# Optimization experiments

Measured on AMD Instinct MI355X. Metric: run time of the kernel, lower is better.

The kernel has to match this reference:

```python
import jax, jax.numpy as jnp
import numpy as np

B, S, H, UNITS = 32, 2048, 1024, 1024


def setup_inputs() -> dict:
    key = jax.random.key(0)
    ks = jax.random.split(key, 5)
    scale = 1.0 / np.sqrt(H)
    return {
        "query": jax.random.normal(ks[0], (B, H), dtype=jnp.float32),
        "values": jax.random.normal(ks[1], (B, S, H), dtype=jnp.float32),
        "W1": jax.random.normal(ks[2], (H, UNITS), dtype=jnp.float32) * scale,
        "b1": jnp.zeros((UNITS,), dtype=jnp.float32),
        "W2": jax.random.normal(ks[3], (H, UNITS), dtype=jnp.float32) * scale,
        "b2": jnp.zeros((UNITS,), dtype=jnp.float32),
        "V": jax.random.normal(ks[4], (UNITS, 1), dtype=jnp.float32) * (1.0 / np.sqrt(UNITS)),
        "bV": jnp.zeros((1,), dtype=jnp.float32),
    }


def reference(query, values, W1, b1, W2, b2, V, bV):
    # W1(values): [B,S,U]; W2(query): [B,1,U] broadcast over S
    proj_v = jnp.einsum("bsh,hu->bsu", values, W1) + b1
    proj_q = (query @ W2 + b2)[:, None, :]
    score = jnp.tanh(proj_v + proj_q) @ V + bV          # [B,S,1]
    attention_weights = jax.nn.softmax(score, axis=1)   # softmax over seq
    context_vector = jnp.sum(attention_weights * values, axis=1)  # [B,H]
    return (attention_weights, context_vector)
```

## Files before the change

### kernel.cpp

```cpp
#include <hip/hip_runtime.h>
#include <hip/hip_bf16.h>
#include <stdint.h>

#define B_ 32
#define S_ 2048
#define H_ 1024
#define U_ 1024

typedef __attribute__((ext_vector_type(8))) short short8;
typedef __attribute__((ext_vector_type(4))) float f32x4;

#define AS1 __attribute__((address_space(1)))
#define AS3 __attribute__((address_space(3)))
#define FENCE __builtin_amdgcn_sched_barrier(0)
#define VMC(n) asm volatile("s_waitcnt vmcnt(" #n ")" ::: "memory")
#define LGKM0 asm volatile("s_waitcnt lgkmcnt(0)" ::: "memory")

__device__ __forceinline__ unsigned short f2bf(float f) {
  unsigned int u = __float_as_uint(f);
  u += 0x7fffu + ((u >> 16) & 1u);
  return (unsigned short)(u >> 16);
}

__global__ void k_transpose_w1(const float* __restrict__ W1, unsigned short* __restrict__ W1T) {
  __shared__ float tile[64][65];
  const int tx = threadIdx.x, ty = threadIdx.y;
  const int u0 = blockIdx.x * 64, h0 = blockIdx.y * 64;
#pragma unroll
  for (int i = 0; i < 16; ++i) {
    int hl = ty + i * 4;
    tile[hl][tx] = W1[(size_t)(h0 + hl) * U_ + (u0 + tx)];
  }
  __syncthreads();
#pragma unroll
  for (int i = 0; i < 16; ++i) {
    int ul = ty + i * 4;
    W1T[(size_t)(u0 + ul) * H_ + (h0 + tx)] = f2bf(tile[tx][ul]);
  }
}

__global__ void k_b1q(const float* __restrict__ query, const float* __restrict__ W2,
                      const float* __restrict__ b1, const float* __restrict__ b2,
                      float* __restrict__ b1q) {
  const int b = blockIdx.y;
  const int u = blockIdx.x * 256 + threadIdx.x;
  float acc = b1[u] + b2[u];
  const float* q = query + b * H_;
#pragma unroll 8
  for (int h = 0; h < H_; ++h) acc += q[h] * W2[(size_t)h * U_ + u];
  b1q[b * U_ + u] = acc;
}

#define BMT 256
#define BNT 256
#define BKT 64
#define NTILE 16

__global__ __launch_bounds__(512, 2)
void k_fused_score(const float* __restrict__ values, const unsigned short* __restrict__ W1T,
                   const float* __restrict__ b1q, const float* __restrict__ V,
                   float* __restrict__ score_part) {
  __shared__ __align__(16) unsigned char smem[131072];
  unsigned short* Abuf = (unsigned short*)smem;
  unsigned short* Bbuf = (unsigned short*)(smem + 65536);
  float* scorebuf = (float*)smem;

  const int tid = threadIdx.x;
  const int g = blockIdx.x;
  const int seq = (g & 7) * 128 + (g >> 3);
  const int bn = seq & 3;
  const int bm = seq >> 2;

  const int lane = tid & 63, wid = tid >> 6;
  const int wm = wid >> 2, wn = wid & 3;
  const int u0 = bn * BNT;

  const int arow = tid >> 2;
  const int acp  = (tid & 3) * 2;
  const float* aBase = values + (size_t)(bm * BMT) * H_;

  const int l15 = lane & 15, l16 = lane >> 4, l7 = lane & 7;
  const int pA0 = (wm * 128 + l15) * 64 + ((0 + l16) ^ l7) * 8;
  const int pA1 = (wm * 128 + l15) * 64 + ((4 + l16) ^ l7) * 8;
  const int pB0 = (wn * 64 + l15) * 64 + ((0 + l16) ^ l7) * 8;
  const int pB1 = (wn * 64 + l15) * 64 + ((4 + l16) ^ l7) * 8;

  f32x4 acc[8][4];
#pragma unroll
  for (int mf = 0; mf < 8; ++mf)
#pragma unroll
    for (int nf = 0; nf < 4; ++nf) acc[mf][nf] = (f32x4){0.f, 0.f, 0.f, 0.f};

  float4 ar0[4], ar1[4];
  short8 af[4], bfv[8];

#define ISSUE_A(reg, tt, h) { \
    const float4* ap_ = (const float4*)(aBase + (size_t)((h) * 128 + arow) * H_ + (tt) * 64 + acp * 8); \
    reg[0] = ap_[0]; reg[1] = ap_[1]; reg[2] = ap_[2]; reg[3] = ap_[3]; }

#define ISSUE_B(tt, dd, h) { \
    _Pragma("unroll") \
    for (int j_ = 0; j_ < 2; ++j_) { \
      const int pbase_ = (h) * 1024 + (wid * 2 + j_) * 64; \
      const int p_ = pbase_ + lane; \
      const int nr_ = p_ >> 3; \
      const int lc_ = (p_ & 7) ^ (nr_ & 7); \
      const unsigned short* src_ = W1T + (size_t)(u0 + nr_) * H_ + (tt) * 64 + lc_ * 8; \
      __builtin_amdgcn_global_load_lds((const AS1 void*)src_, (AS3 void*)&Bbuf[(dd) * 16384 + pbase_ * 8], 16, 0, 0); } }

#define WRITE_A(reg, dd, h) { \
    short8 w0_, w1_; \
    w0_[0]=f2bf(reg[0].x); w0_[1]=f2bf(reg[0].y); w0_[2]=f2bf(reg[0].z); w0_[3]=f2bf(reg[0].w); \
    w0_[4]=f2bf(reg[1].x); w0_[5]=f2bf(reg[1].y); w0_[6]=f2bf(reg[1].z); w0_[7]=f2bf(reg[1].w); \
    w1_[0]=f2bf(reg[2].x); w1_[1]=f2bf(reg[2].y); w1_[2]=f2bf(reg[2].z); w1_[3]=f2bf(reg[2].w); \
    w1_[4]=f2bf(reg[3].x); w1_[5]=f2bf(reg[3].y); w1_[6]=f2bf(reg[3].z); w1_[7]=f2bf(reg[3].w); \
    const int rl_ = (h) * 128 + arow; \
    *(short8*)&Abuf[(dd) * 16384 + rl_ * 64 + ((acp ^ (rl_ & 7)) << 3)] = w0_; \
    *(short8*)&Abuf[(dd) * 16384 + rl_ * 64 + (((acp + 1) ^ (rl_ & 7)) << 3)] = w1_; }

#define READ_AF(q) \
    af[0] = *(const short8*)&Abuf[dA + pA0 + (2 * (q) + 0) * 1024]; \
    af[1] = *(const short8*)&Abuf[dA + pA1 + (2 * (q) + 0) * 1024]; \
    af[2] = *(const short8*)&Abuf[dA + pA0 + (2 * (q) + 1) * 1024]; \
    af[3] = *(const short8*)&Abuf[dA + pA1 + (2 * (q) + 1) * 1024];

#define PHASE_TAIL(q) \
    FENCE; \
    __builtin_amdgcn_s_barrier(); \
    LGKM0; \
    FENCE; \
    __builtin_amdgcn_s_setprio(1); \
    _Pragma("unroll") \
    for (int nf_ = 0; nf_ < 4; ++nf_) { \
      acc[2*(q)+0][nf_] = __builtin_amdgcn_mfma_f32_16x16x32_bf16(af[0], bfv[2*nf_+0], acc[2*(q)+0][nf_], 0, 0, 0); \
      acc[2*(q)+0][nf_] = __builtin_amdgcn_mfma_f32_16x16x32_bf16(af[1], bfv[2*nf_+1], acc[2*(q)+0][nf_], 0, 0, 0); \
      acc[2*(q)+1][nf_] = __builtin_amdgcn_mfma_f32_16x16x32_bf16(af[2], bfv[2*nf_+0], acc[2*(q)+1][nf_], 0, 0, 0); \
      acc[2*(q)+1][nf_] = __builtin_amdgcn_mfma_f32_16x16x32_bf16(af[3], bfv[2*nf_+1], acc[2*(q)+1][nf_], 0, 0, 0); \
    } \
    __builtin_amdgcn_s_setprio(0); \
    FENCE; \
    __builtin_amdgcn_s_barrier();

  ISSUE_A(ar0, 0, 0);
  ISSUE_A(ar1, 0, 1);
  ISSUE_B(0, 0, 0);
  ISSUE_B(0, 0, 1);
  VMC(8);  WRITE_A(ar0, 0, 0);
  VMC(4);  WRITE_A(ar1, 0, 1);
  FENCE;
  ISSUE_A(ar0, 1, 0);
  FENCE;
  VMC(4);
  LGKM0;
  __builtin_amdgcn_s_barrier();

  for (int t = 0; t < NTILE; ++t) {
    const int d = t & 1, dn = d ^ 1;
    const int n  = (t + 1 < NTILE) ? (t + 1) : (NTILE - 1);
    const int n2 = (t + 2 < NTILE) ? (t + 2) : (NTILE - 1);
    const int dA = d * 16384;
    const int dB = d * 16384;

    READ_AF(0);
    bfv[0] = *(const short8*)&Bbuf[dB + pB0 + 0 * 1024];
    bfv[1] = *(const short8*)&Bbuf[dB + pB1 + 0 * 1024];
    bfv[2] = *(const short8*)&Bbuf[dB + pB0 + 1 * 1024];
    bfv[3] = *(const short8*)&Bbuf[dB + pB1 + 1 * 1024];
    bfv[4] = *(const short8*)&Bbuf[dB + pB0 + 2 * 1024];
    bfv[5] = *(const short8*)&Bbuf[dB + pB1 + 2 * 1024];
    bfv[6] = *(const short8*)&Bbuf[dB + pB0 + 3 * 1024];
    bfv[7] = *(const short8*)&Bbuf[dB + pB1 + 3 * 1024];
    ISSUE_A(ar1, n, 1);
    ISSUE_B(n, dn, 0);
    PHASE_TAIL(0);

    READ_AF(1);
    ISSUE_B(n, dn, 1);
    PHASE_TAIL(1);

    READ_AF(2);
    VMC(8);
    WRITE_A(ar0, dn, 0);
    PHASE_TAIL(2);

    READ_AF(3);
    VMC(4);
    WRITE_A(ar1, dn, 1);
    FENCE;
    ISSUE_A(ar0, n2, 0);
    FENCE;
    VMC(4);
    PHASE_TAIL(3);
  }

  __syncthreads();
  const int b_blk = bm >> 3;
  float bqv[4], vvv[4];
#pragma unroll
  for (int nf = 0; nf < 4; ++nf) {
    const int ug = u0 + wn * 64 + nf * 16 + l15;
    bqv[nf] = b1q[b_blk * U_ + ug];
    vvv[nf] = V[ug];
  }
  float rp[8][4];
#pragma unroll
  for (int mf = 0; mf < 8; ++mf)
#pragma unroll
    for (int j = 0; j < 4; ++j) rp[mf][j] = 0.f;
#pragma unroll
  for (int nf = 0; nf < 4; ++nf)
#pragma unroll
    for (int mf = 0; mf < 8; ++mf) {
      const f32x4 c = acc[mf][nf];
#pragma unroll
      for (int j = 0; j < 4; ++j) {
        const float x = c[j] + bqv[nf];
        const float e = __expf(2.f * x);
        const float tt = 1.f - 2.f / (e + 1.f);
        rp[mf][j] += tt * vvv[nf];
      }
    }
#pragma unroll
  for (int mf = 0; mf < 8; ++mf)
#pragma unroll
    for (int j = 0; j < 4; ++j) {
      float v = rp[mf][j];
      v += __shfl_xor(v, 1);
      v += __shfl_xor(v, 2);
      v += __shfl_xor(v, 4);
      v += __shfl_xor(v, 8);
      rp[mf][j] = v;
    }
  if (l15 == 0) {
#pragma unroll
    for (int mf = 0; mf < 8; ++mf)
#pragma unroll
      for (int j = 0; j < 4; ++j)
        scorebuf[(wm * 128 + mf * 16 + l16 * 4 + j) * 4 + wn] = rp[mf][j];
  }
  __syncthreads();
  if (tid < BMT) {
    const float s = scorebuf[tid * 4 + 0] + scorebuf[tid * 4 + 1] +
                    scorebuf[tid * 4 + 2] + scorebuf[tid * 4 + 3];
    score_part[(size_t)bn * (B_ * S_) + bm * BMT + tid] = s;
  }
}

__global__ void k_softmax(const float* __restrict__ sp, float* __restrict__ aw) {
  __shared__ float red[8];
  const int b = blockIdx.x, tid = threadIdx.x;
  const int BS = B_ * S_;
  float x[8];
  float m = -1e30f;
#pragma unroll
  for (int i = 0; i < 8; ++i) {
    const int s = b * S_ + tid + i * 256;
    x[i] = sp[s] + sp[BS + s] + sp[2 * BS + s] + sp[3 * BS + s];
    m = fmaxf(m, x[i]);
  }
#pragma unroll
  for (int off = 32; off; off >>= 1) m = fmaxf(m, __shfl_xor(m, off));
  if ((tid & 63) == 0) red[tid >> 6] = m;
  __syncthreads();
  m = fmaxf(fmaxf(red[0], red[1]), fmaxf(red[2], red[3]));
  float e[8];
  float sum = 0.f;
#pragma unroll
  for (int i = 0; i < 8; ++i) { e[i] = __expf(x[i] - m); sum += e[i]; }
#pragma unroll
  for (int off = 32; off; off >>= 1) sum += __shfl_xor(sum, off);
  __syncthreads();
  if ((tid & 63) == 0) red[4 + (tid >> 6)] = sum;
  __syncthreads();
  sum = red[4] + red[5] + red[6] + red[7];
  const float inv = 1.f / sum;
#pragma unroll
  for (int i = 0; i < 8; ++i) aw[b * S_ + tid + i * 256] = e[i] * inv;
}

__global__ void k_ctx_partial(const float* __restrict__ values, const float* __restrict__ aw,
                              float* __restrict__ part) {
  __shared__ float a_s[128];
  const int b = blockIdx.y, sc = blockIdx.x, tid = threadIdx.x;
  if (tid < 128) a_s[tid] = aw[b * S_ + sc * 128 + tid];
  __syncthreads();
  const float4* vp = (const float4*)values + (size_t)(b * S_ + sc * 128) * (H_ / 4) + tid;
  float4 acc = {0.f, 0.f, 0.f, 0.f};
#pragma unroll 4
  for (int i = 0; i < 128; ++i) {
    const float4 v = vp[(size_t)i * (H_ / 4)];
    const float a = a_s[i];
    acc.x += a * v.x; acc.y += a * v.y; acc.z += a * v.z; acc.w += a * v.w;
  }
  ((float4*)part)[(size_t)(b * 16 + sc) * (H_ / 4) + tid] = acc;
}

__global__ void k_ctx_combine(const float* __restrict__ part, float* __restrict__ ctx) {
  const int b = blockIdx.x, tid = threadIdx.x;
  float4 s = {0.f, 0.f, 0.f, 0.f};
#pragma unroll
  for (int c = 0; c < 16; ++c) {
    const float4 v = ((const float4*)part)[(size_t)(b * 16 + c) * (H_ / 4) + tid];
    s.x += v.x; s.y += v.y; s.z += v.z; s.w += v.w;
  }
  ((float4*)ctx)[b * (H_ / 4) + tid] = s;
}

extern "C" void kernel_launch(void* const* d_in, const int* in_sizes, int n_in,
                              void* d_out, int out_size, void* d_ws, size_t ws_size,
                              hipStream_t stream) {
  const float* query  = (const float*)d_in[0];
  const float* values = (const float*)d_in[1];
  const float* W1     = (const float*)d_in[2];
  const float* b1     = (const float*)d_in[3];
  const float* W2     = (const float*)d_in[4];
  const float* b2     = (const float*)d_in[5];
  const float* V      = (const float*)d_in[6];

  char* ws = (char*)d_ws;
  unsigned short* W1T = (unsigned short*)ws;
  float* b1q   = (float*)(ws + 2u * 1024u * 1024u);
  float* spart = (float*)(ws + 2u * 1024u * 1024u + 128u * 1024u);
  float* cpart = (float*)(ws + 2u * 1024u * 1024u + 128u * 1024u + 1024u * 1024u);

  float* aw  = (float*)d_out;
  float* ctx = aw + B_ * S_;

  hipLaunchKernelGGL(k_transpose_w1, dim3(16, 16), dim3(64, 4), 0, stream, W1, W1T);
  hipLaunchKernelGGL(k_b1q,          dim3(4, 32),  dim3(256),   0, stream, query, W2, b1, b2, b1q);
  hipLaunchKernelGGL(k_fused_score,  dim3(1024),   dim3(512),   0, stream, values, W1T, b1q, V, spart);
  hipLaunchKernelGGL(k_softmax,      dim3(32),     dim3(256),   0, stream, spart, aw);
  hipLaunchKernelGGL(k_ctx_partial,  dim3(16, 32), dim3(256),   0, stream, values, aw, cpart);
  hipLaunchKernelGGL(k_ctx_combine,  dim3(32),     dim3(256),   0, stream, cpart, ctx);
}
```

Baseline: 343.7 us.

## Pre-convert values to bf16 and stage A tiles via direct global-to-LDS loads

When the workspace is large enough, a separate kernel converts the full values tensor to bf16. The GEMM then loads A tiles straight into LDS with global_load_lds, like B, instead of loading fp32 into registers and converting. The MFMA phase ordering is also restructured to reuse B fragments across four M fragments. This adds a full extra pass over values (256MB read plus 128MB write) in exchange for halving GEMM A traffic and removing in-loop conversion. Whether that path runs depends on the workspace size.

```diff
diff --git a/kernel.cpp b/kernel.cpp
--- a/kernel.cpp
+++ b/kernel.cpp
@@ -20,6 +20,18 @@
   unsigned int u = __float_as_uint(f);
   u += 0x7fffu + ((u >> 16) & 1u);
   return (unsigned short)(u >> 16);
+}
+
+__global__ void k_cvt(const float* __restrict__ v, unsigned short* __restrict__ o) {
+  const size_t n = (size_t)B_ * S_ * H_;
+  const size_t stride = (size_t)gridDim.x * blockDim.x * 8;
+  for (size_t i = ((size_t)blockIdx.x * blockDim.x + threadIdx.x) * 8; i < n; i += stride) {
+    float4 a = *(const float4*)(v + i), b = *(const float4*)(v + i + 4);
+    short8 w;
+    w[0]=f2bf(a.x); w[1]=f2bf(a.y); w[2]=f2bf(a.z); w[3]=f2bf(a.w);
+    w[4]=f2bf(b.x); w[5]=f2bf(b.y); w[6]=f2bf(b.z); w[7]=f2bf(b.w);
+    *(short8*)(o + i) = w;
+  }
 }
 
 __global__ void k_transpose_w1(const float* __restrict__ W1, unsigned short* __restrict__ W1T) {
@@ -53,13 +65,13 @@
 
 #define BMT 256
 #define BNT 256
-#define BKT 64
 #define NTILE 16
 
+template<bool CVT>
 __global__ __launch_bounds__(512, 2)
-void k_fused_score(const float* __restrict__ values, const unsigned short* __restrict__ W1T,
-                   const float* __restrict__ b1q, const float* __restrict__ V,
-                   float* __restrict__ score_part) {
+void k_fused_score(const float* __restrict__ valsf, const unsigned short* __restrict__ vbf,
+                   const unsigned short* __restrict__ W1T, const float* __restrict__ b1q,
+                   const float* __restrict__ V, float* __restrict__ score_part) {
   __shared__ __align__(16) unsigned char smem[131072];
   unsigned short* Abuf = (unsigned short*)smem;
   unsigned short* Bbuf = (unsigned short*)(smem + 65536);
@@ -75,16 +87,15 @@
   const int wm = wid >> 2, wn = wid & 3;
   const int u0 = bn * BNT;
 
-  const int arow = tid >> 2;
-  const int acp  = (tid & 3) * 2;
-  const float* aBase = values + (size_t)(bm * BMT) * H_;
-
   const int l15 = lane & 15, l16 = lane >> 4, l7 = lane & 7;
   const int pA0 = (wm * 128 + l15) * 64 + ((0 + l16) ^ l7) * 8;
   const int pA1 = (wm * 128 + l15) * 64 + ((4 + l16) ^ l7) * 8;
   const int pB0 = (wn * 64 + l15) * 64 + ((0 + l16) ^ l7) * 8;
   const int pB1 = (wn * 64 + l15) * 64 + ((4 + l16) ^ l7) * 8;
 
+  const int lcs = (lane & 7) ^ ((lane >> 3) & 7);
+  const int arow = tid >> 2, acp = (tid & 3) * 2;
+
   f32x4 acc[8][4];
 #pragma unroll
   for (int mf = 0; mf < 8; ++mf)
@@ -92,23 +103,29 @@
     for (int nf = 0; nf < 4; ++nf) acc[mf][nf] = (f32x4){0.f, 0.f, 0.f, 0.f};
 
   float4 ar0[4], ar1[4];
-  short8 af[4], bfv[8];
-
-#define ISSUE_A(reg, tt, h) { \
-    const float4* ap_ = (const float4*)(aBase + (size_t)((h) * 128 + arow) * H_ + (tt) * 64 + acp * 8); \
-    reg[0] = ap_[0]; reg[1] = ap_[1]; reg[2] = ap_[2]; reg[3] = ap_[3]; }
-
-#define ISSUE_B(tt, dd, h) { \
+  short8 af_[4], bv[4];
+
+#define STAGE_A(tt, dd, h) { \
     _Pragma("unroll") \
     for (int j_ = 0; j_ < 2; ++j_) { \
-      const int pbase_ = (h) * 1024 + (wid * 2 + j_) * 64; \
-      const int p_ = pbase_ + lane; \
+      const int p_ = (h) * 1024 + (wid * 2 + j_) * 64 + lane; \
       const int nr_ = p_ >> 3; \
-      const int lc_ = (p_ & 7) ^ (nr_ & 7); \
-      const unsigned short* src_ = W1T + (size_t)(u0 + nr_) * H_ + (tt) * 64 + lc_ * 8; \
-      __builtin_amdgcn_global_load_lds((const AS1 void*)src_, (AS3 void*)&Bbuf[(dd) * 16384 + pbase_ * 8], 16, 0, 0); } }
-
-#define WRITE_A(reg, dd, h) { \
+      const unsigned short* s_ = vbf + (size_t)(bm * BMT + nr_) * H_ + (tt) * 64 + lcs * 8; \
+      __builtin_amdgcn_global_load_lds((const AS1 void*)s_, (AS3 void*)&Abuf[(dd) * 16384 + p_ * 8], 16, 0, 0); } }
+
+#define STAGE_B(tt, dd, h) { \
+    _Pragma("unroll") \
+    for (int j_ = 0; j_ < 2; ++j_) { \
+      const int p_ = (h) * 1024 + (wid * 2 + j_) * 64 + lane; \
+      const int nr_ = p_ >> 3; \
+      const unsigned short* s_ = W1T + (size_t)(u0 + nr_) * H_ + (tt) * 64 + lcs * 8; \
+      __builtin_amdgcn_global_load_lds((const AS1 void*)s_, (AS3 void*)&Bbuf[(dd) * 16384 + p_ * 8], 16, 0, 0); } }
+
+#define ISSUE_AR(reg, tt, h) { \
+    const float4* ap_ = (const float4*)(valsf + (size_t)(bm * BMT + (h) * 128 + arow) * H_ + (tt) * 64 + acp * 8); \
+    reg[0] = ap_[0]; reg[1] = ap_[1]; reg[2] = ap_[2]; reg[3] = ap_[3]; }
+
+#define WRITE_AR(reg, dd, h) { \
     short8 w0_, w1_; \
     w0_[0]=f2bf(reg[0].x); w0_[1]=f2bf(reg[0].y); w0_[2]=f2bf(reg[0].z); w0_[3]=f2bf(reg[0].w); \
     w0_[4]=f2bf(reg[1].x); w0_[5]=f2bf(reg[1].y); w0_[6]=f2bf(reg[1].z); w0_[7]=f2bf(reg[1].w); \
@@ -118,79 +135,84 @@
     *(short8*)&Abuf[(dd) * 16384 + rl_ * 64 + ((acp ^ (rl_ & 7)) << 3)] = w0_; \
     *(short8*)&Abuf[(dd) * 16384 + rl_ * 64 + (((acp + 1) ^ (rl_ & 7)) << 3)] = w1_; }
 
-#define READ_AF(q) \
-    af[0] = *(const short8*)&Abuf[dA + pA0 + (2 * (q) + 0) * 1024]; \
-    af[1] = *(const short8*)&Abuf[dA + pA1 + (2 * (q) + 0) * 1024]; \
-    af[2] = *(const short8*)&Abuf[dA + pA0 + (2 * (q) + 1) * 1024]; \
-    af[3] = *(const short8*)&Abuf[dA + pA1 + (2 * (q) + 1) * 1024];
-
-#define PHASE_TAIL(q) \
-    FENCE; \
-    __builtin_amdgcn_s_barrier(); \
-    LGKM0; \
-    FENCE; \
-    __builtin_amdgcn_s_setprio(1); \
+#define READ_AF(PA, MH) \
+    af_[0] = *(const short8*)&Abuf[dA + (PA) + ((MH) * 4 + 0) * 1024]; \
+    af_[1] = *(const short8*)&Abuf[dA + (PA) + ((MH) * 4 + 1) * 1024]; \
+    af_[2] = *(const short8*)&Abuf[dA + (PA) + ((MH) * 4 + 2) * 1024]; \
+    af_[3] = *(const short8*)&Abuf[dA + (PA) + ((MH) * 4 + 3) * 1024];
+
+#define READ_BV(PB) \
+    bv[0] = *(const short8*)&Bbuf[dB + (PB)]; \
+    bv[1] = *(const short8*)&Bbuf[dB + (PB) + 1024]; \
+    bv[2] = *(const short8*)&Bbuf[dB + (PB) + 2048]; \
+    bv[3] = *(const short8*)&Bbuf[dB + (PB) + 3072];
+
+#define MFMA16(MH) \
     _Pragma("unroll") \
     for (int nf_ = 0; nf_ < 4; ++nf_) { \
-      acc[2*(q)+0][nf_] = __builtin_amdgcn_mfma_f32_16x16x32_bf16(af[0], bfv[2*nf_+0], acc[2*(q)+0][nf_], 0, 0, 0); \
-      acc[2*(q)+0][nf_] = __builtin_amdgcn_mfma_f32_16x16x32_bf16(af[1], bfv[2*nf_+1], acc[2*(q)+0][nf_], 0, 0, 0); \
-      acc[2*(q)+1][nf_] = __builtin_amdgcn_mfma_f32_16x16x32_bf16(af[2], bfv[2*nf_+0], acc[2*(q)+1][nf_], 0, 0, 0); \
-      acc[2*(q)+1][nf_] = __builtin_amdgcn_mfma_f32_16x16x32_bf16(af[3], bfv[2*nf_+1], acc[2*(q)+1][nf_], 0, 0, 0); \
-    } \
-    __builtin_amdgcn_s_setprio(0); \
-    FENCE; \
+      acc[(MH)*4+0][nf_] = __builtin_amdgcn_mfma_f32_16x16x32_bf16(af_[0], bv[nf_], acc[(MH)*4+0][nf_], 0, 0, 0); \
+      acc[(MH)*4+1][nf_] = __builtin_amdgcn_mfma_f32_16x16x32_bf16(af_[1], bv[nf_], acc[(MH)*4+1][nf_], 0, 0, 0); \
+      acc[(MH)*4+2][nf_] = __builtin_amdgcn_mfma_f32_16x16x32_bf16(af_[2], bv[nf_], acc[(MH)*4+2][nf_], 0, 0, 0); \
+      acc[(MH)*4+3][nf_] = __builtin_amdgcn_mfma_f32_16x16x32_bf16(af_[3], bv[nf_], acc[(MH)*4+3][nf_], 0, 0, 0); \
+    }
+
+#define PH_HEAD FENCE; __builtin_amdgcn_s_barrier(); LGKM0; FENCE; __builtin_amdgcn_s_setprio(1)
+#define PH_MID  __builtin_amdgcn_s_setprio(0)
+#define PH_END  FENCE; __builtin_amdgcn_s_barrier()
+
+  if constexpr (CVT) {
+    STAGE_A(0, 0, 0); STAGE_A(0, 0, 1);
+    STAGE_B(0, 0, 0); STAGE_B(0, 0, 1);
+    VMC(0);
     __builtin_amdgcn_s_barrier();
-
-  ISSUE_A(ar0, 0, 0);
-  ISSUE_A(ar1, 0, 1);
-  ISSUE_B(0, 0, 0);
-  ISSUE_B(0, 0, 1);
-  VMC(8);  WRITE_A(ar0, 0, 0);
-  VMC(4);  WRITE_A(ar1, 0, 1);
-  FENCE;
-  ISSUE_A(ar0, 1, 0);
-  FENCE;
-  VMC(4);
-  LGKM0;
-  __builtin_amdgcn_s_barrier();
+    STAGE_B(1, 1, 0);
+  } else {
+    ISSUE_AR(ar0, 0, 0); ISSUE_AR(ar1, 0, 1);
+    STAGE_B(0, 0, 0); STAGE_B(0, 0, 1);
+    VMC(8);  WRITE_AR(ar0, 0, 0);
+    VMC(4);  WRITE_AR(ar1, 0, 1);
+    FENCE;
+    ISSUE_AR(ar0, 1, 0); ISSUE_AR(ar1, 1, 1);
+    FENCE;
+    VMC(8);
+    LGKM0;
+    __builtin_amdgcn_s_barrier();
+  }
 
   for (int t = 0; t < NTILE; ++t) {
     const int d = t & 1, dn = d ^ 1;
-    const int n  = (t + 1 < NTILE) ? (t + 1) : (NTILE - 1);
-    const int n2 = (t + 2 < NTILE) ? (t + 2) : (NTILE - 1);
-    const int dA = d * 16384;
-    const int dB = d * 16384;
-
-    READ_AF(0);
-    bfv[0] = *(const short8*)&Bbuf[dB + pB0 + 0 * 1024];
-    bfv[1] = *(const short8*)&Bbuf[dB + pB1 + 0 * 1024];
-    bfv[2] = *(const short8*)&Bbuf[dB + pB0 + 1 * 1024];
-    bfv[3] = *(const short8*)&Bbuf[dB + pB1 + 1 * 1024];
-    bfv[4] = *(const short8*)&Bbuf[dB + pB0 + 2 * 1024];
-    bfv[5] = *(const short8*)&Bbuf[dB + pB1 + 2 * 1024];
-    bfv[6] = *(const short8*)&Bbuf[dB + pB0 + 3 * 1024];
-    bfv[7] = *(const short8*)&Bbuf[dB + pB1 + 3 * 1024];
-    ISSUE_A(ar1, n, 1);
-    ISSUE_B(n, dn, 0);
-    PHASE_TAIL(0);
-
-    READ_AF(1);
-    ISSUE_B(n, dn, 1);
-    PHASE_TAIL(1);
-
-    READ_AF(2);
-    VMC(8);
-    WRITE_A(ar0, dn, 0);
-    PHASE_TAIL(2);
-
-    READ_AF(3);
-    VMC(4);
-    WRITE_A(ar1, dn, 1);
-    FENCE;
-    ISSUE_A(ar0, n2, 0);
-    FENCE;
-    VMC(4);
-    PHASE_TAIL(3);
+    const int dA = d * 16384, dB = d * 16384;
+    const int n  = (t + 1 < NTILE) ? t + 1 : NTILE - 1;
+    const int n2 = (t + 2 < NTILE) ? t + 2 : NTILE - 1;
+
+    READ_BV(pB0);
+    READ_AF(pA0, 0);
+    if constexpr (CVT) { STAGE_A(n, dn, 0); } else { STAGE_B(n, dn, 0); }
+    PH_HEAD; MFMA16(0); PH_MID; PH_END;
+
+    READ_AF(pA0, 1);
+    if constexpr (CVT) { STAGE_A(n, dn, 1); } else { STAGE_B(n, dn, 1); }
+    PH_HEAD; MFMA16(1); PH_MID; PH_END;
+
+    READ_BV(pB1);
+    READ_AF(pA1, 0);
+    if constexpr (CVT) { STAGE_B(n, dn, 1); }
+    else { VMC(8); WRITE_AR(ar0, dn, 0); }
+    PH_HEAD; MFMA16(0); PH_MID; PH_END;
+
+    READ_AF(pA1, 1);
+    if constexpr (!CVT) { VMC(4); WRITE_AR(ar1, dn, 1); }
+    PH_HEAD; MFMA16(1); PH_MID;
+    if constexpr (CVT) {
+      STAGE_B(n2, d, 0);
+      VMC(2);
+    } else {
+      FENCE;
+      ISSUE_AR(ar0, n2, 0); ISSUE_AR(ar1, n2, 1);
+      FENCE;
+      VMC(8);
+    }
+    PH_END;
   }
 
   __syncthreads();
@@ -322,14 +344,21 @@
   float* b1q   = (float*)(ws + 2u * 1024u * 1024u);
   float* spart = (float*)(ws + 2u * 1024u * 1024u + 128u * 1024u);
   float* cpart = (float*)(ws + 2u * 1024u * 1024u + 128u * 1024u + 1024u * 1024u);
+  unsigned short* vbf = (unsigned short*)(ws + 8u * 1024u * 1024u);
+  const bool useCvt = ws_size >= (size_t)136 * 1024 * 1024;
 
   float* aw  = (float*)d_out;
   float* ctx = aw + B_ * S_;
 
-  hipLaunchKernelGGL(k_transpose_w1, dim3(16, 16), dim3(64, 4), 0, stream, W1, W1T);
-  hipLaunchKernelGGL(k_b1q,          dim3(4, 32),  dim3(256),   0, stream, query, W2, b1, b2, b1q);
-  hipLaunchKernelGGL(k_fused_score,  dim3(1024),   dim3(512),   0, stream, values, W1T, b1q, V, spart);
-  hipLaunchKernelGGL(k_softmax,      dim3(32),     dim3(256),   0, stream, spart, aw);
-  hipLaunchKernelGGL(k_ctx_partial,  dim3(16, 32), dim3(256),   0, stream, values, aw, cpart);
-  hipLaunchKernelGGL(k_ctx_combine,  dim3(32),     dim3(256),   0, stream, cpart, ctx);
-}
+  k_transpose_w1<<<dim3(16, 16), dim3(64, 4), 0, stream>>>(W1, W1T);
+  k_b1q<<<dim3(4, 32), dim3(256), 0, stream>>>(query, W2, b1, b2, b1q);
+  if (useCvt) {
+    k_cvt<<<dim3(2048), dim3(256), 0, stream>>>(values, vbf);
+    k_fused_score<true><<<dim3(1024), dim3(512), 0, stream>>>(values, vbf, W1T, b1q, V, spart);
+  } else {
+    k_fused_score<false><<<dim3(1024), dim3(512), 0, stream>>>(values, vbf, W1T, b1q, V, spart);
+  }
+  k_softmax<<<dim3(32), dim3(256), 0, stream>>>(spart, aw);
+  k_ctx_partial<<<dim3(16, 32), dim3(256), 0, stream>>>(values, aw, cpart);
+  k_ctx_combine<<<dim3(32), dim3(256), 0, stream>>>(cpart, ctx);
+}
```

New measurement: 333.3 us. -3.0%, faster.
